# Optimization experiments

Hardware: AMD Instinct MI355X
Metric: run time of the kernel (lower is better)

Reference implementation:

```python
import jax, jax.numpy as jnp
import numpy as np

B, S, HIDDEN = 2, 2048, 2048
H, KVH, HD = 16, 4, 128
N_REP = H // KVH
WIN = 3  # hardcoded window_size in the module
ROPE_THETA = 10000.0


def _rope(x, cos, sin):
    # x: [b, s, h, d]; cos/sin: [s, d//2]. Pairs are consecutive elements
    # (view_as_complex on reshape(..., -1, 2)): a = even idx, b = odd idx.
    a = x[..., 0::2]
    b = x[..., 1::2]
    c = cos[None, :, None, :]
    s = sin[None, :, None, :]
    out = jnp.stack([a * c - b * s, a * s + b * c], axis=-1)  # [b,s,h,d//2,2]
    return out.reshape(x.shape)


def setup_inputs() -> dict:
    key = jax.random.key(0)
    ks = jax.random.split(key, 5)
    x = jax.random.normal(ks[0], (B, S, HIDDEN), dtype=jnp.float32)
    scale = 0.02
    wq = jax.random.normal(ks[1], (HIDDEN, H * HD), dtype=jnp.float32) * scale
    wk = jax.random.normal(ks[2], (HIDDEN, KVH * HD), dtype=jnp.float32) * scale
    wv = jax.random.normal(ks[3], (HIDDEN, KVH * HD), dtype=jnp.float32) * scale
    wo = jax.random.normal(ks[4], (H * HD, HIDDEN), dtype=jnp.float32) * scale
    # Standard RoPE angles (equivalent to the complex freqs_cis)
    inv_freq = 1.0 / (ROPE_THETA ** (np.arange(0, HD, 2, dtype=np.float64) / HD))
    ang = np.outer(np.arange(S, dtype=np.float64), inv_freq)  # [S, HD//2]
    cos = jnp.asarray(np.cos(ang), dtype=jnp.float32)
    sin = jnp.asarray(np.sin(ang), dtype=jnp.float32)
    return {"x": x, "wq": wq, "wk": wk, "wv": wv, "wo": wo, "cos": cos, "sin": sin}


def reference(x, wq, wk, wv, wo, cos, sin):
    q = (x @ wq).reshape(B, S, H, HD)
    k = (x @ wk).reshape(B, S, KVH, HD)
    v = (x @ wv).reshape(B, S, KVH, HD)
    q = _rope(q, cos, sin)
    k = _rope(k, cos, sin)
    # GQA: repeat kv heads (repeat_kv)
    k = jnp.repeat(k, N_REP, axis=2)  # [B,S,H,HD]
    v = jnp.repeat(v, N_REP, axis=2)
    scores = jnp.einsum("bqhd,bkhd->bhqk", q, k) / np.float32(np.sqrt(HD))
    i = jnp.arange(S)[:, None]
    j = jnp.arange(S)[None, :]
    allowed = (j <= i) & (j > i - WIN)
    scores = jnp.where(allowed, scores, -jnp.inf)
    attn = jax.nn.softmax(scores.astype(jnp.float32), axis=-1).astype(q.dtype)
    out = jnp.einsum("bhqk,bkhd->bqhd", attn, v).reshape(B, S, H * HD)
    return (out @ wo, attn)
```

## Files before the change

### kernel.cpp

```cpp
#include <hip/hip_runtime.h>

#define SEQ 2048
#define HID 2048
#define NH 16
#define NKVH 4
#define HDIM 128
#define NB 2
#define MTOT (NB * SEQ)
#define QKV_N (NH * HDIM + 2 * NKVH * HDIM)
#define OUT0_ELEMS (NB * SEQ * HID)
#define ATTN_ELEMS ((size_t)NB * NH * SEQ * SEQ)
#define ATTN_CHUNKS (ATTN_ELEMS / 4)
#define Z1_CHUNK 26048
#define Z1_TOTAL ((long)768 * Z1_CHUNK)
#define Z2_CHUNK 26464

typedef __bf16 bf16x8 __attribute__((ext_vector_type(8)));
typedef float f32x4 __attribute__((ext_vector_type(4)));

__device__ __forceinline__ unsigned short f2bf(float f) {
  unsigned int u = __float_as_uint(f);
  u += 0x7FFFu + ((u >> 16) & 1u);
  return (unsigned short)(u >> 16);
}
__device__ __forceinline__ float bf2f(unsigned short u) {
  return __uint_as_float(((unsigned int)u) << 16);
}

__global__ void cvt_f32_bf16_k(const float* __restrict__ in,
                               unsigned short* __restrict__ out, int n4) {
  int stride = gridDim.x * blockDim.x;
  for (int i = blockIdx.x * blockDim.x + threadIdx.x; i < n4; i += stride) {
    float4 v = ((const float4*)in)[i];
    ushort4 o;
    o.x = f2bf(v.x); o.y = f2bf(v.y); o.z = f2bf(v.z); o.w = f2bf(v.w);
    ((ushort4*)out)[i] = o;
  }
}

__global__ void transpose_cvt_k(const float* __restrict__ W,
                                unsigned short* __restrict__ Wt, int K, int N) {
  __shared__ float tile[32][33];
  int n0 = blockIdx.x * 32, k0 = blockIdx.y * 32;
  int tx = threadIdx.x, ty = threadIdx.y;
  #pragma unroll
  for (int r = 0; r < 32; r += 8)
    tile[ty + r][tx] = W[(size_t)(k0 + ty + r) * N + n0 + tx];
  __syncthreads();
  #pragma unroll
  for (int r = 0; r < 32; r += 8)
    Wt[(size_t)(n0 + ty + r) * K + k0 + tx] = f2bf(tile[tx][ty + r]);
}

template <bool OUT_BF16>
__global__ __launch_bounds__(256) void gemm_bt_k(
    const unsigned short* __restrict__ A, const unsigned short* __restrict__ Bt,
    void* __restrict__ Cv, int M, int N, int K,
    f32x4* __restrict__ attn4, long zoff, int zchunk) {
  __shared__ unsigned short As[128 * 32];
  __shared__ unsigned short Bs[128 * 32];
  const int t = threadIdx.x;
  const int row0 = blockIdx.y << 7;
  const int col0 = blockIdx.x << 7;
  const int lane = t & 63;
  const int wave = t >> 6;
  const int wr = (wave >> 1) << 6;
  const int wc = (wave & 1) << 6;
  const int lrow = lane & 15;
  const int kofs = (lane >> 4) << 3;

  const long zbase = zoff + (long)(blockIdx.y * gridDim.x + blockIdx.x) * zchunk;

  f32x4 acc[4][4];
  #pragma unroll
  for (int a = 0; a < 4; ++a)
    #pragma unroll
    for (int b = 0; b < 4; ++b)
      #pragma unroll
      for (int r = 0; r < 4; ++r) acc[a][b][r] = 0.f;

  const int ar0 = t >> 2, ac0 = (t & 3) << 3;
  const int ar1 = ar0 + 64;

  const unsigned short* Ab = A + (size_t)row0 * K;
  const unsigned short* Bb = Bt + (size_t)col0 * K;

  const int nk = K >> 5;
  for (int kt = 0; kt < nk; ++kt) {
    const int k0 = kt << 5;
    if (kt) __syncthreads();
    __builtin_amdgcn_global_load_lds(
        (const __attribute__((address_space(1))) void*)(Ab + (size_t)ar0 * K + k0 + ac0),
        (__attribute__((address_space(3))) void*)(As + t * 8), 16, 0, 0);
    __builtin_amdgcn_global_load_lds(
        (const __attribute__((address_space(1))) void*)(Ab + (size_t)ar1 * K + k0 + ac0),
        (__attribute__((address_space(3))) void*)(As + (t + 256) * 8), 16, 0, 0);
    __builtin_amdgcn_global_load_lds(
        (const __attribute__((address_space(1))) void*)(Bb + (size_t)ar0 * K + k0 + ac0),
        (__attribute__((address_space(3))) void*)(Bs + t * 8), 16, 0, 0);
    __builtin_amdgcn_global_load_lds(
        (const __attribute__((address_space(1))) void*)(Bb + (size_t)ar1 * K + k0 + ac0),
        (__attribute__((address_space(3))) void*)(Bs + (t + 256) * 8), 16, 0, 0);

    #pragma unroll
    for (int s = 0; s < 2; ++s) {
      int il = (kt * 2 + s) * 256 + t;
      if (il < zchunk) {
        long g = zbase + il;
        int c = (int)(g & 511);
        int i = (int)((g >> 9) & (SEQ - 1));
        int hi = i >> 2;
        int lo = (i >= 2 ? i - 2 : 0) >> 2;
        if (c != hi && c != lo) {
          f32x4 z = {0.f, 0.f, 0.f, 0.f};
          __builtin_nontemporal_store(z, attn4 + g);
        }
      }
    }
    __syncthreads();

    bf16x8 af[4], bfr[4];
    #pragma unroll
    for (int mf = 0; mf < 4; ++mf)
      af[mf] = *(const bf16x8*)(As + ((wr + mf * 16 + lrow) << 5) + kofs);
    #pragma unroll
    for (int nf = 0; nf < 4; ++nf)
      bfr[nf] = *(const bf16x8*)(Bs + ((wc + nf * 16 + lrow) << 5) + kofs);
    #pragma unroll
    for (int mf = 0; mf < 4; ++mf)
      #pragma unroll
      for (int nf = 0; nf < 4; ++nf)
        acc[mf][nf] = __builtin_amdgcn_mfma_f32_16x16x32_bf16(af[mf], bfr[nf],
                                                              acc[mf][nf], 0, 0, 0);
  }

  const int cr = row0 + wr + ((lane >> 4) << 2);
  const int cc = col0 + wc + (lane & 15);
  #pragma unroll
  for (int mf = 0; mf < 4; ++mf)
    #pragma unroll
    for (int nf = 0; nf < 4; ++nf)
      #pragma unroll
      for (int r = 0; r < 4; ++r) {
        size_t idx = (size_t)(cr + mf * 16 + r) * N + cc + nf * 16;
        if constexpr (OUT_BF16)
          ((unsigned short*)Cv)[idx] = f2bf(acc[mf][nf][r]);
        else
          ((float*)Cv)[idx] = acc[mf][nf][r];
      }
}

__device__ __forceinline__ float rope_val(float v, int lane, float c, float s) {
  float p = __shfl_xor(v, 1, 64);
  return (lane & 1) ? (p * s + v * c) : (v * c - p * s);
}

__global__ void attn_k(const unsigned short* __restrict__ QKV,
                       unsigned short* __restrict__ AO,
                       float* __restrict__ attn_out,
                       const float* __restrict__ cosT,
                       const float* __restrict__ sinT) {
  int unit = blockIdx.x * 4 + (threadIdx.x >> 6);
  int lane = threadIdx.x & 63;
  int h = unit & (NH - 1);
  int mi = unit >> 4;
  int i = mi & (SEQ - 1);
  int kh = h >> 2;
  const float SCALE = 0.08838834764831845f;
  const int tt = lane >> 1;

  const unsigned short* qp = QKV + (size_t)mi * QKV_N + h * HDIM;
  float ci0 = cosT[i * 64 + tt],      si0 = sinT[i * 64 + tt];
  float ci1 = cosT[i * 64 + 32 + tt], si1 = sinT[i * 64 + 32 + tt];
  float q0 = rope_val(bf2f(qp[lane]),      lane, ci0, si0);
  float q1 = rope_val(bf2f(qp[lane + 64]), lane, ci1, si1);

  float sc[3];
  #pragma unroll
  for (int jj = 0; jj < 3; ++jj) {
    int j = i - 2 + jj;
    float d = -1e30f;
    if (j >= 0) {
      const unsigned short* kp = QKV + (size_t)(mi - i + j) * QKV_N + 2048 + kh * HDIM;
      float cj0 = cosT[j * 64 + tt],      sj0 = sinT[j * 64 + tt];
      float cj1 = cosT[j * 64 + 32 + tt], sj1 = sinT[j * 64 + 32 + tt];
      float k0 = rope_val(bf2f(kp[lane]),      lane, cj0, sj0);
      float k1 = rope_val(bf2f(kp[lane + 64]), lane, cj1, sj1);
      float part = q0 * k0 + q1 * k1;
      #pragma unroll
      for (int o = 32; o; o >>= 1) part += __shfl_xor(part, o, 64);
      d = part * SCALE;
    }
    sc[jj] = d;
  }
  float mx = fmaxf(fmaxf(sc[0], sc[1]), sc[2]);
  float p0 = __expf(sc[0] - mx), p1 = __expf(sc[1] - mx), p2 = __expf(sc[2] - mx);
  float inv = 1.0f / (p0 + p1 + p2);
  float aw[3] = {p0 * inv, p1 * inv, p2 * inv};

  float o0 = 0.f, o1 = 0.f;
  #pragma unroll
  for (int jj = 0; jj < 3; ++jj) {
    int j = i - 2 + jj;
    if (j >= 0) {
      const unsigned short* vp = QKV + (size_t)(mi - i + j) * QKV_N + 2560 + kh * HDIM;
      o0 += aw[jj] * bf2f(vp[lane]);
      o1 += aw[jj] * bf2f(vp[lane + 64]);
    }
  }
  size_t ao_base = (size_t)mi * HID + h * HDIM;
  AO[ao_base + lane] = f2bf(o0);
  AO[ao_base + lane + 64] = f2bf(o1);

  int b = mi >> 11;
  int rowg = (b * NH + h) * SEQ + i;
  int lo = (i >= 2 ? i - 2 : 0) >> 2;
  int hi = i >> 2;
  if (lane == 0 || (lane == 1 && hi != lo)) {
    int c = (lane == 0) ? lo : hi;
    f32x4 val = {0.f, 0.f, 0.f, 0.f};
    #pragma unroll
    for (int q = 0; q < 4; ++q) {
      int j = c * 4 + q;
      int d = j - (i - 2);
      if (d >= 0 && d < 3 && j <= i) val[q] = aw[d];
    }
    __builtin_nontemporal_store(val, (f32x4*)(attn_out + (size_t)rowg * SEQ) + c);
  }
}

extern "C" void kernel_launch(void* const* d_in, const int* in_sizes, int n_in,
                              void* d_out, int out_size, void* d_ws, size_t ws_size,
                              hipStream_t stream) {
  const float* x    = (const float*)d_in[0];
  const float* wq   = (const float*)d_in[1];
  const float* wk   = (const float*)d_in[2];
  const float* wv   = (const float*)d_in[3];
  const float* wo   = (const float*)d_in[4];
  const float* cosT = (const float*)d_in[5];
  const float* sinT = (const float*)d_in[6];

  float* out  = (float*)d_out;
  float* attn = out + OUT0_ELEMS;

  char* ws = (char*)d_ws;
  unsigned short* Xbf   = (unsigned short*)ws;  ws += (size_t)MTOT * HID * 2;
  unsigned short* Wqkvt = (unsigned short*)ws;  ws += (size_t)QKV_N * HID * 2;
  unsigned short* Wot   = (unsigned short*)ws;  ws += (size_t)HID * HID * 2;
  unsigned short* QKV   = (unsigned short*)ws;  ws += (size_t)MTOT * QKV_N * 2;
  unsigned short* AO    = (unsigned short*)ws;


  cvt_f32_bf16_k<<<2048, 256, 0, stream>>>(x, Xbf, MTOT * HID / 4);

  dim3 tb(32, 8);
  transpose_cvt_k<<<dim3(64, 64), tb, 0, stream>>>(wq, Wqkvt, HID, 2048);
  transpose_cvt_k<<<dim3(16, 64), tb, 0, stream>>>(wk, Wqkvt + (size_t)2048 * HID, HID, 512);
  transpose_cvt_k<<<dim3(16, 64), tb, 0, stream>>>(wv, Wqkvt + (size_t)2560 * HID, HID, 512);
  transpose_cvt_k<<<dim3(64, 64), tb, 0, stream>>>(wo, Wot, HID, 2048);

  gemm_bt_k<true><<<dim3(QKV_N / 128, MTOT / 128), 256, 0, stream>>>(
      Xbf, Wqkvt, QKV, MTOT, QKV_N, HID, (f32x4*)attn, 0L, Z1_CHUNK);

  attn_k<<<MTOT * NH / 4, 256, 0, stream>>>(QKV, AO, attn, cosT, sinT);

  gemm_bt_k<false><<<dim3(HID / 128, MTOT / 128), 256, 0, stream>>>(
      AO, Wot, out, MTOT, HID, HID, (f32x4*)attn, Z1_TOTAL, Z2_CHUNK);
}
```

Measured before the change: 210.0 us.

## Fuse prep kernels, add XCD-aware block swizzle, overlap zero-fill with LDS reads

Merges the x conversion and the four weight transpose-convert launches into one prep kernel, cutting four kernel launches and their gaps. Remaps GEMM block IDs so consecutive blocks spread across the 8 XCDs in contiguous tile groups, aiming for better L2 locality. Moves the LDS barrier and fragment reads ahead of the attn zero-fill stores so those stores overlap with the shared-memory loads. The zero-fill chunk mapping stays tied to the raw block id, so coverage is unchanged.

```diff
diff --git a/kernel.cpp b/kernel.cpp
--- a/kernel.cpp
+++ b/kernel.cpp
@@ -10,7 +10,6 @@
 #define QKV_N (NH * HDIM + 2 * NKVH * HDIM)
 #define OUT0_ELEMS (NB * SEQ * HID)
 #define ATTN_ELEMS ((size_t)NB * NH * SEQ * SEQ)
-#define ATTN_CHUNKS (ATTN_ELEMS / 4)
 #define Z1_CHUNK 26048
 #define Z1_TOTAL ((long)768 * Z1_CHUNK)
 #define Z2_CHUNK 26464
@@ -27,29 +26,36 @@
   return __uint_as_float(((unsigned int)u) << 16);
 }
 
-__global__ void cvt_f32_bf16_k(const float* __restrict__ in,
-                               unsigned short* __restrict__ out, int n4) {
-  int stride = gridDim.x * blockDim.x;
-  for (int i = blockIdx.x * blockDim.x + threadIdx.x; i < n4; i += stride) {
-    float4 v = ((const float4*)in)[i];
+__global__ __launch_bounds__(256) void prep_k(
+    const float* __restrict__ x, const float* __restrict__ wq,
+    const float* __restrict__ wk, const float* __restrict__ wv,
+    const float* __restrict__ wo, unsigned short* __restrict__ Xbf,
+    unsigned short* __restrict__ Wqkvt, unsigned short* __restrict__ Wot) {
+  __shared__ float tile[32][33];
+  const int bid = blockIdx.x, t = threadIdx.x;
+  if (bid < 8192) {
+    int i = bid * 256 + t;
+    float4 v = ((const float4*)x)[i];
     ushort4 o;
     o.x = f2bf(v.x); o.y = f2bf(v.y); o.z = f2bf(v.z); o.w = f2bf(v.w);
-    ((ushort4*)out)[i] = o;
-  }
-}
-
-__global__ void transpose_cvt_k(const float* __restrict__ W,
-                                unsigned short* __restrict__ Wt, int K, int N) {
-  __shared__ float tile[32][33];
-  int n0 = blockIdx.x * 32, k0 = blockIdx.y * 32;
-  int tx = threadIdx.x, ty = threadIdx.y;
+    ((ushort4*)Xbf)[i] = o;
+    return;
+  }
+  int lb = bid - 8192;
+  const float* W; unsigned short* Wt; int gx, N;
+  if (lb < 4096)      { W = wq; Wt = Wqkvt;                       gx = 64; N = 2048; }
+  else if (lb < 5120) { W = wk; Wt = Wqkvt + (size_t)2048 * HID;  gx = 16; N = 512;  lb -= 4096; }
+  else if (lb < 6144) { W = wv; Wt = Wqkvt + (size_t)2560 * HID;  gx = 16; N = 512;  lb -= 5120; }
+  else                { W = wo; Wt = Wot;                         gx = 64; N = 2048; lb -= 6144; }
+  const int n0 = (lb % gx) * 32, k0 = (lb / gx) * 32;
+  const int tx = t & 31, ty = t >> 5;
   #pragma unroll
   for (int r = 0; r < 32; r += 8)
     tile[ty + r][tx] = W[(size_t)(k0 + ty + r) * N + n0 + tx];
   __syncthreads();
   #pragma unroll
   for (int r = 0; r < 32; r += 8)
-    Wt[(size_t)(n0 + ty + r) * K + k0 + tx] = f2bf(tile[tx][ty + r]);
+    Wt[(size_t)(n0 + ty + r) * HID + k0 + tx] = f2bf(tile[tx][ty + r]);
 }
 
 template <bool OUT_BF16>
@@ -60,8 +66,12 @@
   __shared__ unsigned short As[128 * 32];
   __shared__ unsigned short Bs[128 * 32];
   const int t = threadIdx.x;
-  const int row0 = blockIdx.y << 7;
-  const int col0 = blockIdx.x << 7;
+  const int nbx = gridDim.x;
+  const int rawbid = blockIdx.y * nbx + blockIdx.x;
+  const int nwg = nbx * gridDim.y;
+  const int sw = (rawbid & 7) * (nwg >> 3) + (rawbid >> 3);
+  const int row0 = (sw / nbx) << 7;
+  const int col0 = (sw % nbx) << 7;
   const int lane = t & 63;
   const int wave = t >> 6;
   const int wr = (wave >> 1) << 6;
@@ -69,7 +79,7 @@
   const int lrow = lane & 15;
   const int kofs = (lane >> 4) << 3;
 
-  const long zbase = zoff + (long)(blockIdx.y * gridDim.x + blockIdx.x) * zchunk;
+  const long zbase = zoff + (long)rawbid * zchunk;
 
   f32x4 acc[4][4];
   #pragma unroll
@@ -101,6 +111,15 @@
     __builtin_amdgcn_global_load_lds(
         (const __attribute__((address_space(1))) void*)(Bb + (size_t)ar1 * K + k0 + ac0),
         (__attribute__((address_space(3))) void*)(Bs + (t + 256) * 8), 16, 0, 0);
+    __syncthreads();
+
+    bf16x8 af[4], bfr[4];
+    #pragma unroll
+    for (int mf = 0; mf < 4; ++mf)
+      af[mf] = *(const bf16x8*)(As + ((wr + mf * 16 + lrow) << 5) + kofs);
+    #pragma unroll
+    for (int nf = 0; nf < 4; ++nf)
+      bfr[nf] = *(const bf16x8*)(Bs + ((wc + nf * 16 + lrow) << 5) + kofs);
 
     #pragma unroll
     for (int s = 0; s < 2; ++s) {
@@ -117,15 +136,7 @@
         }
       }
     }
-    __syncthreads();
-
-    bf16x8 af[4], bfr[4];
-    #pragma unroll
-    for (int mf = 0; mf < 4; ++mf)
-      af[mf] = *(const bf16x8*)(As + ((wr + mf * 16 + lrow) << 5) + kofs);
-    #pragma unroll
-    for (int nf = 0; nf < 4; ++nf)
-      bfr[nf] = *(const bf16x8*)(Bs + ((wc + nf * 16 + lrow) << 5) + kofs);
+
     #pragma unroll
     for (int mf = 0; mf < 4; ++mf)
       #pragma unroll
@@ -250,14 +261,7 @@
   unsigned short* QKV   = (unsigned short*)ws;  ws += (size_t)MTOT * QKV_N * 2;
   unsigned short* AO    = (unsigned short*)ws;
 
-
-  cvt_f32_bf16_k<<<2048, 256, 0, stream>>>(x, Xbf, MTOT * HID / 4);
-
-  dim3 tb(32, 8);
-  transpose_cvt_k<<<dim3(64, 64), tb, 0, stream>>>(wq, Wqkvt, HID, 2048);
-  transpose_cvt_k<<<dim3(16, 64), tb, 0, stream>>>(wk, Wqkvt + (size_t)2048 * HID, HID, 512);
-  transpose_cvt_k<<<dim3(16, 64), tb, 0, stream>>>(wv, Wqkvt + (size_t)2560 * HID, HID, 512);
-  transpose_cvt_k<<<dim3(64, 64), tb, 0, stream>>>(wo, Wot, HID, 2048);
+  prep_k<<<18432, 256, 0, stream>>>(x, wq, wk, wv, wo, Xbf, Wqkvt, Wot);
 
   gemm_bt_k<true><<<dim3(QKV_N / 128, MTOT / 128), 256, 0, stream>>>(
       Xbf, Wqkvt, QKV, MTOT, QKV_N, HID, (f32x4*)attn, 0L, Z1_CHUNK);
```

Measured after the change: 197.3 us. 1.06x faster.
